# Kernel tuning notes

Hardware: AMD Instinct MI355X
Metric: run time of the kernel (lower is better)

The kernel has to match this reference:

```python
import jax, jax.numpy as jnp
import numpy as np

N_NODES = 100000
N_EDGES = 1600000
IN_CH = 128


def _sage_conv(x, src, dst, Wl, b, Wr, n_nodes):
    # PyG SAGEConv (aggr='mean', root_weight=True):
    #   out_i = lin_l(mean_{j->i} x_j) + lin_r(x_i)
    msg = x[src]                                             # [E, F]
    agg = jax.ops.segment_sum(msg, dst, num_segments=n_nodes)  # [N, F]
    deg = jax.ops.segment_sum(jnp.ones((src.shape[0],), x.dtype), dst,
                              num_segments=n_nodes)          # [N]
    mean = agg / jnp.maximum(deg, 1.0)[:, None]
    return mean @ Wl + b + x @ Wr


def setup_inputs() -> dict:
    key = jax.random.key(0)
    ks = jax.random.split(key, 10)
    x = jax.random.normal(ks[0], (N_NODES, IN_CH), dtype=jnp.float32)
    edge_index = jax.random.randint(ks[1], (2, N_EDGES), 0, N_NODES, dtype=jnp.int64)
    s = 0.05
    return {
        "x": x,
        "edge_index": edge_index,
        "W1l": jax.random.normal(ks[2], (IN_CH, 32), dtype=jnp.float32) * s,
        "b1": jax.random.normal(ks[3], (32,), dtype=jnp.float32) * s,
        "W1r": jax.random.normal(ks[4], (IN_CH, 32), dtype=jnp.float32) * s,
        "W2l": jax.random.normal(ks[5], (32, 16), dtype=jnp.float32) * s,
        "b2": jax.random.normal(ks[6], (16,), dtype=jnp.float32) * s,
        "W2r": jax.random.normal(ks[7], (32, 16), dtype=jnp.float32) * s,
        "Wfc": jax.random.normal(ks[8], (16, 2), dtype=jnp.float32) * s,
        "bfc": jax.random.normal(ks[9], (2,), dtype=jnp.float32) * s,
    }


def reference(x, edge_index, W1l, b1, W1r, W2l, b2, W2r, Wfc, bfc):
    src, dst = edge_index[0], edge_index[1]
    n = x.shape[0]
    h = jax.nn.relu(_sage_conv(x, src, dst, W1l, b1, W1r, n))   # [N, 32]
    h = jax.nn.relu(_sage_conv(h, src, dst, W2l, b2, W2r, n))   # [N, 16]
    return h @ Wfc + bfc                                        # [N, 2]
```

## Files before the change

### kernel.cpp

```cpp
#include <hip/hip_runtime.h>

#define TPB 256
#define BK_SHIFT 7
#define BK_SIZE 128
#define NBK_MAX 800
#define EPT 32

typedef __attribute__((ext_vector_type(8))) short bf16x8;
typedef __attribute__((ext_vector_type(4))) float f32x4;

__device__ __forceinline__ unsigned short f2bf(float f) {
    unsigned u = __float_as_uint(f);
    unsigned r = (u + 0x7FFFu + ((u >> 16) & 1u)) >> 16;
    return (unsigned short)r;
}
__device__ __forceinline__ float bf2f(unsigned short b) {
    return __uint_as_float((unsigned)b << 16);
}

__global__ __launch_bounds__(256) void hist_buckets(
    const int* __restrict__ dst, int* __restrict__ bcnt, int E, int NBK)
{
    __shared__ int h[NBK_MAX];
    const int t = threadIdx.x;
    for (int i = t; i < NBK; i += 256) h[i] = 0;
    __syncthreads();
    const int E4 = E >> 2;
    for (int e4 = blockIdx.x * blockDim.x + t; e4 < E4; e4 += gridDim.x * blockDim.x) {
        int4 d = ((const int4*)dst)[e4];
        atomicAdd(&h[d.x >> BK_SHIFT], 1);
        atomicAdd(&h[d.y >> BK_SHIFT], 1);
        atomicAdd(&h[d.z >> BK_SHIFT], 1);
        atomicAdd(&h[d.w >> BK_SHIFT], 1);
    }
    if (blockIdx.x == 0) {
        for (int e = E4 * 4 + t; e < E; e += 256)
            atomicAdd(&h[dst[e] >> BK_SHIFT], 1);
    }
    __syncthreads();
    for (int i = t; i < NBK; i += 256)
        if (h[i]) atomicAdd(&bcnt[i], h[i]);
}

__global__ __launch_bounds__(1024) void scan_buckets(
    const int* __restrict__ bcnt, int* __restrict__ bbase,
    int* __restrict__ gcursor, int NBK)
{
    __shared__ int s[1024];
    const int t = threadIdx.x;
    int v = (t < NBK) ? bcnt[t] : 0;
    s[t] = v;
    __syncthreads();
    for (int off = 1; off < 1024; off <<= 1) {
        int u = (t >= off) ? s[t - off] : 0;
        __syncthreads();
        s[t] += u;
        __syncthreads();
    }
    if (t < NBK) {
        int excl = s[t] - v;
        bbase[t]   = excl;
        gcursor[t] = excl;
    }
}

__global__ __launch_bounds__(256) void bin_scatter(
    const int* __restrict__ src, const int* __restrict__ dst,
    int* __restrict__ gcursor, int* __restrict__ pk, int E, int NBK)
{
    __shared__ int lcnt[NBK_MAX];
    __shared__ int lbase[NBK_MAX];
    __shared__ int lrank[NBK_MAX];
    const int t = threadIdx.x;
    const int e0 = blockIdx.x * (256 * EPT);

    for (int i = t; i < NBK; i += 256) { lcnt[i] = 0; lrank[i] = 0; }
    __syncthreads();

    #pragma unroll 4
    for (int k = 0; k < EPT; ++k) {
        int e = e0 + k * 256 + t;
        if (e < E) atomicAdd(&lcnt[dst[e] >> BK_SHIFT], 1);
    }
    __syncthreads();

    for (int i = t; i < NBK; i += 256) {
        int c = lcnt[i];
        if (c) lbase[i] = atomicAdd(&gcursor[i], c);
    }
    __syncthreads();

    #pragma unroll 4
    for (int k = 0; k < EPT; ++k) {
        int e = e0 + k * 256 + t;
        if (e < E) {
            int d = dst[e], s = src[e];
            int b = d >> BK_SHIFT;
            int r = atomicAdd(&lrank[b], 1);
            pk[lbase[b] + r] = (s << BK_SHIFT) | (d & (BK_SIZE - 1));
        }
    }
}

__global__ __launch_bounds__(256) void bucket_csr(
    const int* __restrict__ pk, const int* __restrict__ bbase,
    const int* __restrict__ bcnt,
    int* __restrict__ csr_src, int* __restrict__ row_start,
    int* __restrict__ row_end, int N)
{
    __shared__ int lcnt[BK_SIZE];
    __shared__ int s[BK_SIZE];
    __shared__ int wcur[BK_SIZE];
    const int t = threadIdx.x;
    const int b = blockIdx.x;
    const int base = bbase[b];
    const int cnt  = bcnt[b];
    const int node0 = b * BK_SIZE;

    if (t < BK_SIZE) lcnt[t] = 0;
    __syncthreads();

    for (int j = t; j < cnt; j += 256)
        atomicAdd(&lcnt[pk[base + j] & (BK_SIZE - 1)], 1);
    __syncthreads();

    if (t < BK_SIZE) s[t] = lcnt[t];
    __syncthreads();
    for (int off = 1; off < BK_SIZE; off <<= 1) {
        int u = (t < BK_SIZE && t >= off) ? s[t - off] : 0;
        __syncthreads();
        if (t < BK_SIZE) s[t] += u;
        __syncthreads();
    }
    if (t < BK_SIZE) {
        int excl = s[t] - lcnt[t];
        wcur[t] = excl;
        int node = node0 + t;
        if (node < N) {
            row_start[node] = base + excl;
            row_end[node]   = base + s[t];
        }
    }
    __syncthreads();

    for (int j = t; j < cnt; j += 256) {
        int v = pk[base + j];
        int d = v & (BK_SIZE - 1);
        int pos = atomicAdd(&wcur[d], 1);
        csr_src[base + pos] = v >> BK_SHIFT;
    }
}

__global__ __launch_bounds__(256) void gemm1_mfma(
    const float* __restrict__ A,
    const float* __restrict__ Wl,
    const float* __restrict__ Wr,
    const float* __restrict__ b,
    unsigned short* __restrict__ Yb,
    float* __restrict__ C,
    int N)
{
    const int lane = threadIdx.x & 63;
    const int m    = lane & 15;
    const int quad = lane >> 4;
    const int wave   = blockIdx.x * (blockDim.x >> 6) + (threadIdx.x >> 6);
    const int nwaves = gridDim.x * (blockDim.x >> 6);
    const int ntiles = (N + 15) >> 4;

    bf16x8 Bf[4][4];
    #pragma unroll
    for (int kc = 0; kc < 4; ++kc) {
        #pragma unroll
        for (int jt = 0; jt < 4; ++jt) {
            const float* W = (jt < 2) ? Wl : Wr;
            const int col = (jt & 1) * 16 + m;
            #pragma unroll
            for (int j = 0; j < 8; ++j) {
                int k = kc * 32 + quad * 8 + j;
                Bf[kc][jt][j] = (short)f2bf(W[k * 32 + col]);
            }
        }
    }

    const float bias0 = b[m];
    const float bias1 = b[16 + m];

    for (int tile = wave; tile < ntiles; tile += nwaves) {
        const int node0 = tile * 16;
        const int gn = node0 + m;
        const bool okA = gn < N;
        const float* rowp = A + (size_t)gn * 128;

        bf16x8 Af[4];
        #pragma unroll
        for (int kc = 0; kc < 4; ++kc) {
            float4 v0 = make_float4(0.f, 0.f, 0.f, 0.f);
            float4 v1 = make_float4(0.f, 0.f, 0.f, 0.f);
            if (okA) {
                v0 = *(const float4*)&rowp[kc * 32 + quad * 8];
                v1 = *(const float4*)&rowp[kc * 32 + quad * 8 + 4];
            }
            Af[kc][0] = (short)f2bf(v0.x); Af[kc][1] = (short)f2bf(v0.y);
            Af[kc][2] = (short)f2bf(v0.z); Af[kc][3] = (short)f2bf(v0.w);
            Af[kc][4] = (short)f2bf(v1.x); Af[kc][5] = (short)f2bf(v1.y);
            Af[kc][6] = (short)f2bf(v1.z); Af[kc][7] = (short)f2bf(v1.w);
        }

        f32x4 acc[4] = {{0.f,0.f,0.f,0.f},{0.f,0.f,0.f,0.f},
                        {0.f,0.f,0.f,0.f},{0.f,0.f,0.f,0.f}};
        #pragma unroll
        for (int kc = 0; kc < 4; ++kc) {
            #pragma unroll
            for (int jt = 0; jt < 4; ++jt)
                acc[jt] = __builtin_amdgcn_mfma_f32_16x16x32_bf16(
                    Af[kc], Bf[kc][jt], acc[jt], 0, 0, 0);
        }

        const int nodeBase = node0 + quad * 4;
        #pragma unroll
        for (int reg = 0; reg < 4; ++reg) {
            const int node = nodeBase + reg;
            if (node < N) {
                Yb[(size_t)node * 32 + m]      = f2bf(acc[0][reg]);
                Yb[(size_t)node * 32 + 16 + m] = f2bf(acc[1][reg]);
                C [(size_t)node * 32 + m]      = acc[2][reg] + bias0;
                C [(size_t)node * 32 + 16 + m] = acc[3][reg] + bias1;
            }
        }
    }
}

__global__ __launch_bounds__(256) void gather_gemm2(
    const int* __restrict__ row_start, const int* __restrict__ row_end,
    const int* __restrict__ csr_src,
    const unsigned short* __restrict__ Yb,
    const float* __restrict__ c1,
    const float* __restrict__ W2l, const float* __restrict__ W2r,
    const float* __restrict__ b2,
    unsigned short* __restrict__ y2b, float* __restrict__ c2, int N)
{
    int gid  = blockIdx.x * blockDim.x + threadIdx.x;
    int node = gid >> 3;
    int q    = gid & 7;
    const bool active = node < N;

    float h[4] = {0.f, 0.f, 0.f, 0.f};
    if (active) {
        int start = row_start[node];
        int end   = row_end[node];
        float w   = 1.0f / fmaxf((float)(end - start), 1.0f);

        float4 a0 = make_float4(0.f, 0.f, 0.f, 0.f);
        float4 a1 = make_float4(0.f, 0.f, 0.f, 0.f);
        float4 a2 = make_float4(0.f, 0.f, 0.f, 0.f);
        float4 a3 = make_float4(0.f, 0.f, 0.f, 0.f);
        int j = start;
        for (; j + 3 < end; j += 4) {
            int s0 = csr_src[j];
            int s1 = csr_src[j + 1];
            int s2 = csr_src[j + 2];
            int s3 = csr_src[j + 3];
            ushort4 v0 = *(const ushort4*)&Yb[(size_t)s0 * 32 + q * 4];
            ushort4 v1 = *(const ushort4*)&Yb[(size_t)s1 * 32 + q * 4];
            ushort4 v2 = *(const ushort4*)&Yb[(size_t)s2 * 32 + q * 4];
            ushort4 v3 = *(const ushort4*)&Yb[(size_t)s3 * 32 + q * 4];
            a0.x += bf2f(v0.x); a0.y += bf2f(v0.y); a0.z += bf2f(v0.z); a0.w += bf2f(v0.w);
            a1.x += bf2f(v1.x); a1.y += bf2f(v1.y); a1.z += bf2f(v1.z); a1.w += bf2f(v1.w);
            a2.x += bf2f(v2.x); a2.y += bf2f(v2.y); a2.z += bf2f(v2.z); a2.w += bf2f(v2.w);
            a3.x += bf2f(v3.x); a3.y += bf2f(v3.y); a3.z += bf2f(v3.z); a3.w += bf2f(v3.w);
        }
        for (; j < end; ++j) {
            int s = csr_src[j];
            ushort4 v = *(const ushort4*)&Yb[(size_t)s * 32 + q * 4];
            a0.x += bf2f(v.x); a0.y += bf2f(v.y); a0.z += bf2f(v.z); a0.w += bf2f(v.w);
        }
        float4 acc;
        acc.x = (a0.x + a1.x) + (a2.x + a3.x);
        acc.y = (a0.y + a1.y) + (a2.y + a3.y);
        acc.z = (a0.z + a1.z) + (a2.z + a3.z);
        acc.w = (a0.w + a1.w) + (a2.w + a3.w);

        float4 c = *(const float4*)&c1[(size_t)node * 32 + q * 4];
        h[0] = fmaxf(c.x + acc.x * w, 0.f);
        h[1] = fmaxf(c.y + acc.y * w, 0.f);
        h[2] = fmaxf(c.z + acc.z * w, 0.f);
        h[3] = fmaxf(c.w + acc.w * w, 0.f);
    }

    const int  j0  = q * 4;
    const bool isY = (j0 < 16);
    const int  jj  = isY ? j0 : (j0 - 16);
    const float* Wb = isY ? W2l : W2r;

    float o0 = 0.f, o1 = 0.f, o2 = 0.f, o3 = 0.f;
    #pragma unroll
    for (int k = 0; k < 32; ++k) {
        float hk = __shfl(h[k & 3], k >> 2, 8);
        float4 wv = *(const float4*)&Wb[k * 16 + jj];
        o0 += hk * wv.x; o1 += hk * wv.y; o2 += hk * wv.z; o3 += hk * wv.w;
    }

    if (active) {
        if (isY) {
            ushort4 r;
            r.x = f2bf(o0); r.y = f2bf(o1); r.z = f2bf(o2); r.w = f2bf(o3);
            *(ushort4*)&y2b[(size_t)node * 16 + jj] = r;
        } else {
            float4 bb = *(const float4*)&b2[jj];
            *(float4*)&c2[(size_t)node * 16 + jj] =
                make_float4(o0 + bb.x, o1 + bb.y, o2 + bb.z, o3 + bb.w);
        }
    }
}

__global__ __launch_bounds__(256) void gather_final(
    const int* __restrict__ row_start, const int* __restrict__ row_end,
    const int* __restrict__ csr_src,
    const unsigned short* __restrict__ Yb,
    const float* __restrict__ c2,
    const float* __restrict__ Wfc,
    const float* __restrict__ bfc,
    float* __restrict__ out, int N)
{
    int gid  = blockIdx.x * blockDim.x + threadIdx.x;
    int node = gid >> 2;
    int q    = gid & 3;
    if (node >= N) return;

    int start = row_start[node];
    int end   = row_end[node];
    float w   = 1.0f / fmaxf((float)(end - start), 1.0f);

    float4 a0 = make_float4(0.f, 0.f, 0.f, 0.f);
    float4 a1 = make_float4(0.f, 0.f, 0.f, 0.f);
    float4 a2 = make_float4(0.f, 0.f, 0.f, 0.f);
    float4 a3 = make_float4(0.f, 0.f, 0.f, 0.f);
    int j = start;
    for (; j + 3 < end; j += 4) {
        int s0 = csr_src[j];
        int s1 = csr_src[j + 1];
        int s2 = csr_src[j + 2];
        int s3 = csr_src[j + 3];
        ushort4 v0 = *(const ushort4*)&Yb[(size_t)s0 * 16 + q * 4];
        ushort4 v1 = *(const ushort4*)&Yb[(size_t)s1 * 16 + q * 4];
        ushort4 v2 = *(const ushort4*)&Yb[(size_t)s2 * 16 + q * 4];
        ushort4 v3 = *(const ushort4*)&Yb[(size_t)s3 * 16 + q * 4];
        a0.x += bf2f(v0.x); a0.y += bf2f(v0.y); a0.z += bf2f(v0.z); a0.w += bf2f(v0.w);
        a1.x += bf2f(v1.x); a1.y += bf2f(v1.y); a1.z += bf2f(v1.z); a1.w += bf2f(v1.w);
        a2.x += bf2f(v2.x); a2.y += bf2f(v2.y); a2.z += bf2f(v2.z); a2.w += bf2f(v2.w);
        a3.x += bf2f(v3.x); a3.y += bf2f(v3.y); a3.z += bf2f(v3.z); a3.w += bf2f(v3.w);
    }
    for (; j < end; ++j) {
        int s = csr_src[j];
        ushort4 v = *(const ushort4*)&Yb[(size_t)s * 16 + q * 4];
        a0.x += bf2f(v.x); a0.y += bf2f(v.y); a0.z += bf2f(v.z); a0.w += bf2f(v.w);
    }
    float4 acc;
    acc.x = (a0.x + a1.x) + (a2.x + a3.x);
    acc.y = (a0.y + a1.y) + (a2.y + a3.y);
    acc.z = (a0.z + a1.z) + (a2.z + a3.z);
    acc.w = (a0.w + a1.w) + (a2.w + a3.w);

    float4 c = *(const float4*)&c2[(size_t)node * 16 + q * 4];
    float h0 = fmaxf(c.x + acc.x * w, 0.f);
    float h1 = fmaxf(c.y + acc.y * w, 0.f);
    float h2 = fmaxf(c.z + acc.z * w, 0.f);
    float h3 = fmaxf(c.w + acc.w * w, 0.f);

    const float* Wq = &Wfc[q * 8];
    float o0 = h0 * Wq[0] + h1 * Wq[2] + h2 * Wq[4] + h3 * Wq[6];
    float o1 = h0 * Wq[1] + h1 * Wq[3] + h2 * Wq[5] + h3 * Wq[7];

    o0 += __shfl_xor(o0, 1); o0 += __shfl_xor(o0, 2);
    o1 += __shfl_xor(o1, 1); o1 += __shfl_xor(o1, 2);

    if (q == 0) ((float2*)out)[node] = make_float2(o0 + bfc[0], o1 + bfc[1]);
}

extern "C" void kernel_launch(void* const* d_in, const int* in_sizes, int n_in,
                              void* d_out, int out_size, void* d_ws, size_t ws_size,
                              hipStream_t stream)
{
    const float* x   = (const float*)d_in[0];
    const int*   ei  = (const int*)d_in[1];
    const float* W1l = (const float*)d_in[2];
    const float* b1  = (const float*)d_in[3];
    const float* W1r = (const float*)d_in[4];
    const float* W2l = (const float*)d_in[5];
    const float* b2  = (const float*)d_in[6];
    const float* W2r = (const float*)d_in[7];
    const float* Wfc = (const float*)d_in[8];
    const float* bfc = (const float*)d_in[9];
    float* out = (float*)d_out;

    const int N = in_sizes[0] / 128;
    const int E = in_sizes[1] / 2;
    const int* src = ei;
    const int* dst = ei + E;

    const int NBK = (N + BK_SIZE - 1) / BK_SIZE;

    int*   bucket_cnt  = (int*)d_ws;
    int*   bucket_base = bucket_cnt + NBK_MAX;
    int*   gcursor     = bucket_base + NBK_MAX;
    int*   row_start   = gcursor + NBK_MAX;
    int*   row_end     = row_start + N;
    int*   csr_src     = row_end + N;
    unsigned short* y1b = (unsigned short*)(csr_src + E);
    float* c1          = (float*)(y1b + (size_t)N * 32);
    unsigned short* y2b = (unsigned short*)(c1 + (size_t)N * 32);
    float* c2          = (float*)(y2b + (size_t)N * 16);
    int*   pk          = (int*)y1b;

    hipMemsetAsync(bucket_cnt, 0, (size_t)NBK * sizeof(int), stream);
    hist_buckets<<<196, 256, 0, stream>>>(dst, bucket_cnt, E, NBK);
    scan_buckets<<<1, 1024, 0, stream>>>(bucket_cnt, bucket_base, gcursor, NBK);
    {
        int nb = (E + 256 * EPT - 1) / (256 * EPT);
        bin_scatter<<<nb, 256, 0, stream>>>(src, dst, gcursor, pk, E, NBK);
    }
    bucket_csr<<<NBK, 256, 0, stream>>>(pk, bucket_base, bucket_cnt,
                                        csr_src, row_start, row_end, N);

    gemm1_mfma<<<256, TPB, 0, stream>>>(x, W1l, W1r, b1, y1b, c1, N);

    gather_gemm2<<<(N * 8 + TPB - 1) / TPB, TPB, 0, stream>>>(
        row_start, row_end, csr_src, y1b, c1, W2l, W2r, b2, y2b, c2, N);

    gather_final<<<(N * 4 + TPB - 1) / TPB, TPB, 0, stream>>>(
        row_start, row_end, csr_src, y2b, c2, Wfc, bfc, out, N);
}
```

Before: 221.9 us.

## Drop per-node CSR build; aggregate bucketed edges with LDS atomics per block

Removes the bucket_csr kernel and the row_start/row_end/csr_src arrays. Each gather kernel now takes one 128-node bucket per block, streams its packed edges, and accumulates neighbour features into padded shared-memory accumulators with float atomics. Degree is counted in the first gather and stored as invdeg for reuse in the second. This saves a kernel launch and a full pass over the edge list. In exchange it relies on LDS atomic throughput, runs only about 782 blocks, and sums in a nondeterministic order.

```diff
diff --git a/kernel.cpp b/kernel.cpp
--- a/kernel.cpp
+++ b/kernel.cpp
@@ -99,55 +99,6 @@
             int r = atomicAdd(&lrank[b], 1);
             pk[lbase[b] + r] = (s << BK_SHIFT) | (d & (BK_SIZE - 1));
         }
-    }
-}
-
-__global__ __launch_bounds__(256) void bucket_csr(
-    const int* __restrict__ pk, const int* __restrict__ bbase,
-    const int* __restrict__ bcnt,
-    int* __restrict__ csr_src, int* __restrict__ row_start,
-    int* __restrict__ row_end, int N)
-{
-    __shared__ int lcnt[BK_SIZE];
-    __shared__ int s[BK_SIZE];
-    __shared__ int wcur[BK_SIZE];
-    const int t = threadIdx.x;
-    const int b = blockIdx.x;
-    const int base = bbase[b];
-    const int cnt  = bcnt[b];
-    const int node0 = b * BK_SIZE;
-
-    if (t < BK_SIZE) lcnt[t] = 0;
-    __syncthreads();
-
-    for (int j = t; j < cnt; j += 256)
-        atomicAdd(&lcnt[pk[base + j] & (BK_SIZE - 1)], 1);
-    __syncthreads();
-
-    if (t < BK_SIZE) s[t] = lcnt[t];
-    __syncthreads();
-    for (int off = 1; off < BK_SIZE; off <<= 1) {
-        int u = (t < BK_SIZE && t >= off) ? s[t - off] : 0;
-        __syncthreads();
-        if (t < BK_SIZE) s[t] += u;
-        __syncthreads();
-    }
-    if (t < BK_SIZE) {
-        int excl = s[t] - lcnt[t];
-        wcur[t] = excl;
-        int node = node0 + t;
-        if (node < N) {
-            row_start[node] = base + excl;
-            row_end[node]   = base + s[t];
-        }
-    }
-    __syncthreads();
-
-    for (int j = t; j < cnt; j += 256) {
-        int v = pk[base + j];
-        int d = v & (BK_SIZE - 1);
-        int pos = atomicAdd(&wcur[d], 1);
-        csr_src[base + pos] = v >> BK_SHIFT;
     }
 }
 
@@ -231,150 +182,152 @@
 }
 
 __global__ __launch_bounds__(256) void gather_gemm2(
-    const int* __restrict__ row_start, const int* __restrict__ row_end,
-    const int* __restrict__ csr_src,
+    const int* __restrict__ bbase, const int* __restrict__ bcnt,
+    const int* __restrict__ pk,
     const unsigned short* __restrict__ Yb,
     const float* __restrict__ c1,
     const float* __restrict__ W2l, const float* __restrict__ W2r,
     const float* __restrict__ b2,
+    float* __restrict__ invdeg,
     unsigned short* __restrict__ y2b, float* __restrict__ c2, int N)
 {
-    int gid  = blockIdx.x * blockDim.x + threadIdx.x;
-    int node = gid >> 3;
-    int q    = gid & 7;
-    const bool active = node < N;
-
-    float h[4] = {0.f, 0.f, 0.f, 0.f};
-    if (active) {
-        int start = row_start[node];
-        int end   = row_end[node];
-        float w   = 1.0f / fmaxf((float)(end - start), 1.0f);
-
-        float4 a0 = make_float4(0.f, 0.f, 0.f, 0.f);
-        float4 a1 = make_float4(0.f, 0.f, 0.f, 0.f);
-        float4 a2 = make_float4(0.f, 0.f, 0.f, 0.f);
-        float4 a3 = make_float4(0.f, 0.f, 0.f, 0.f);
-        int j = start;
-        for (; j + 3 < end; j += 4) {
-            int s0 = csr_src[j];
-            int s1 = csr_src[j + 1];
-            int s2 = csr_src[j + 2];
-            int s3 = csr_src[j + 3];
-            ushort4 v0 = *(const ushort4*)&Yb[(size_t)s0 * 32 + q * 4];
-            ushort4 v1 = *(const ushort4*)&Yb[(size_t)s1 * 32 + q * 4];
-            ushort4 v2 = *(const ushort4*)&Yb[(size_t)s2 * 32 + q * 4];
-            ushort4 v3 = *(const ushort4*)&Yb[(size_t)s3 * 32 + q * 4];
-            a0.x += bf2f(v0.x); a0.y += bf2f(v0.y); a0.z += bf2f(v0.z); a0.w += bf2f(v0.w);
-            a1.x += bf2f(v1.x); a1.y += bf2f(v1.y); a1.z += bf2f(v1.z); a1.w += bf2f(v1.w);
-            a2.x += bf2f(v2.x); a2.y += bf2f(v2.y); a2.z += bf2f(v2.z); a2.w += bf2f(v2.w);
-            a3.x += bf2f(v3.x); a3.y += bf2f(v3.y); a3.z += bf2f(v3.z); a3.w += bf2f(v3.w);
-        }
-        for (; j < end; ++j) {
-            int s = csr_src[j];
-            ushort4 v = *(const ushort4*)&Yb[(size_t)s * 32 + q * 4];
-            a0.x += bf2f(v.x); a0.y += bf2f(v.y); a0.z += bf2f(v.z); a0.w += bf2f(v.w);
-        }
-        float4 acc;
-        acc.x = (a0.x + a1.x) + (a2.x + a3.x);
-        acc.y = (a0.y + a1.y) + (a2.y + a3.y);
-        acc.z = (a0.z + a1.z) + (a2.z + a3.z);
-        acc.w = (a0.w + a1.w) + (a2.w + a3.w);
-
-        float4 c = *(const float4*)&c1[(size_t)node * 32 + q * 4];
-        h[0] = fmaxf(c.x + acc.x * w, 0.f);
-        h[1] = fmaxf(c.y + acc.y * w, 0.f);
-        h[2] = fmaxf(c.z + acc.z * w, 0.f);
-        h[3] = fmaxf(c.w + acc.w * w, 0.f);
-    }
-
-    const int  j0  = q * 4;
-    const bool isY = (j0 < 16);
-    const int  jj  = isY ? j0 : (j0 - 16);
-    const float* Wb = isY ? W2l : W2r;
-
-    float o0 = 0.f, o1 = 0.f, o2 = 0.f, o3 = 0.f;
-    #pragma unroll
-    for (int k = 0; k < 32; ++k) {
-        float hk = __shfl(h[k & 3], k >> 2, 8);
-        float4 wv = *(const float4*)&Wb[k * 16 + jj];
-        o0 += hk * wv.x; o1 += hk * wv.y; o2 += hk * wv.z; o3 += hk * wv.w;
-    }
-
-    if (active) {
-        if (isY) {
-            ushort4 r;
-            r.x = f2bf(o0); r.y = f2bf(o1); r.z = f2bf(o2); r.w = f2bf(o3);
-            *(ushort4*)&y2b[(size_t)node * 16 + jj] = r;
-        } else {
-            float4 bb = *(const float4*)&b2[jj];
-            *(float4*)&c2[(size_t)node * 16 + jj] =
-                make_float4(o0 + bb.x, o1 + bb.y, o2 + bb.z, o3 + bb.w);
+    __shared__ float acc[BK_SIZE * 33];
+    __shared__ int   ldeg[BK_SIZE];
+
+    const int t = threadIdx.x;
+    const int b = blockIdx.x;
+    const int base = bbase[b];
+    const int cnt  = bcnt[b];
+    const int node0 = b * BK_SIZE;
+
+    for (int i = t; i < BK_SIZE * 33; i += 256) acc[i] = 0.f;
+    if (t < BK_SIZE) ldeg[t] = 0;
+    __syncthreads();
+
+    const int sg = t >> 3;
+    const int q  = t & 7;
+
+    for (int e = sg; e < cnt; e += 32) {
+        int pkv = pk[base + e];
+        int s   = pkv >> BK_SHIFT;
+        int dl  = pkv & (BK_SIZE - 1);
+        ushort4 v = *(const ushort4*)&Yb[(size_t)s * 32 + q * 4];
+        float* ap = &acc[dl * 33 + q * 4];
+        atomicAdd(ap + 0, bf2f(v.x));
+        atomicAdd(ap + 1, bf2f(v.y));
+        atomicAdd(ap + 2, bf2f(v.z));
+        atomicAdd(ap + 3, bf2f(v.w));
+        if (q == 0) atomicAdd(&ldeg[dl], 1);
+    }
+    __syncthreads();
+
+    if (t < BK_SIZE) {
+        int node = node0 + t;
+        if (node < N) {
+            float w = 1.0f / fmaxf((float)ldeg[t], 1.0f);
+            invdeg[node] = w;
+            const float* crow = &c1[(size_t)node * 32];
+            #pragma unroll
+            for (int k = 0; k < 32; ++k)
+                acc[t * 33 + k] = fmaxf(crow[k] + acc[t * 33 + k] * w, 0.f);
+        }
+    }
+    __syncthreads();
+
+    {
+        const int node = t & (BK_SIZE - 1);
+        const int part = t >> 7;
+        const int gn = node0 + node;
+        if (gn < N) {
+            const float* W = part ? W2r : W2l;
+            f32x4 o0 = {0,0,0,0}, o1 = {0,0,0,0}, o2 = {0,0,0,0}, o3 = {0,0,0,0};
+            #pragma unroll
+            for (int k = 0; k < 32; ++k) {
+                float hk = acc[node * 33 + k];
+                float4 w0 = *(const float4*)&W[k * 16 + 0];
+                float4 w1 = *(const float4*)&W[k * 16 + 4];
+                float4 w2 = *(const float4*)&W[k * 16 + 8];
+                float4 w3 = *(const float4*)&W[k * 16 + 12];
+                o0[0] += hk * w0.x; o0[1] += hk * w0.y; o0[2] += hk * w0.z; o0[3] += hk * w0.w;
+                o1[0] += hk * w1.x; o1[1] += hk * w1.y; o1[2] += hk * w1.z; o1[3] += hk * w1.w;
+                o2[0] += hk * w2.x; o2[1] += hk * w2.y; o2[2] += hk * w2.z; o2[3] += hk * w2.w;
+                o3[0] += hk * w3.x; o3[1] += hk * w3.y; o3[2] += hk * w3.z; o3[3] += hk * w3.w;
+            }
+            if (part == 0) {
+                ushort4 r0, r1, r2, r3;
+                r0.x = f2bf(o0[0]); r0.y = f2bf(o0[1]); r0.z = f2bf(o0[2]); r0.w = f2bf(o0[3]);
+                r1.x = f2bf(o1[0]); r1.y = f2bf(o1[1]); r1.z = f2bf(o1[2]); r1.w = f2bf(o1[3]);
+                r2.x = f2bf(o2[0]); r2.y = f2bf(o2[1]); r2.z = f2bf(o2[2]); r2.w = f2bf(o2[3]);
+                r3.x = f2bf(o3[0]); r3.y = f2bf(o3[1]); r3.z = f2bf(o3[2]); r3.w = f2bf(o3[3]);
+                ushort4* yp = (ushort4*)&y2b[(size_t)gn * 16];
+                yp[0] = r0; yp[1] = r1; yp[2] = r2; yp[3] = r3;
+            } else {
+                float4* cp = (float4*)&c2[(size_t)gn * 16];
+                float4 bb0 = *(const float4*)&b2[0];
+                float4 bb1 = *(const float4*)&b2[4];
+                float4 bb2 = *(const float4*)&b2[8];
+                float4 bb3 = *(const float4*)&b2[12];
+                cp[0] = make_float4(o0[0]+bb0.x, o0[1]+bb0.y, o0[2]+bb0.z, o0[3]+bb0.w);
+                cp[1] = make_float4(o1[0]+bb1.x, o1[1]+bb1.y, o1[2]+bb1.z, o1[3]+bb1.w);
+                cp[2] = make_float4(o2[0]+bb2.x, o2[1]+bb2.y, o2[2]+bb2.z, o2[3]+bb2.w);
+                cp[3] = make_float4(o3[0]+bb3.x, o3[1]+bb3.y, o3[2]+bb3.z, o3[3]+bb3.w);
+            }
         }
     }
 }
 
 __global__ __launch_bounds__(256) void gather_final(
-    const int* __restrict__ row_start, const int* __restrict__ row_end,
-    const int* __restrict__ csr_src,
+    const int* __restrict__ bbase, const int* __restrict__ bcnt,
+    const int* __restrict__ pk,
     const unsigned short* __restrict__ Yb,
     const float* __restrict__ c2,
+    const float* __restrict__ invdeg,
     const float* __restrict__ Wfc,
     const float* __restrict__ bfc,
     float* __restrict__ out, int N)
 {
-    int gid  = blockIdx.x * blockDim.x + threadIdx.x;
-    int node = gid >> 2;
-    int q    = gid & 3;
-    if (node >= N) return;
-
-    int start = row_start[node];
-    int end   = row_end[node];
-    float w   = 1.0f / fmaxf((float)(end - start), 1.0f);
-
-    float4 a0 = make_float4(0.f, 0.f, 0.f, 0.f);
-    float4 a1 = make_float4(0.f, 0.f, 0.f, 0.f);
-    float4 a2 = make_float4(0.f, 0.f, 0.f, 0.f);
-    float4 a3 = make_float4(0.f, 0.f, 0.f, 0.f);
-    int j = start;
-    for (; j + 3 < end; j += 4) {
-        int s0 = csr_src[j];
-        int s1 = csr_src[j + 1];
-        int s2 = csr_src[j + 2];
-        int s3 = csr_src[j + 3];
-        ushort4 v0 = *(const ushort4*)&Yb[(size_t)s0 * 16 + q * 4];
-        ushort4 v1 = *(const ushort4*)&Yb[(size_t)s1 * 16 + q * 4];
-        ushort4 v2 = *(const ushort4*)&Yb[(size_t)s2 * 16 + q * 4];
-        ushort4 v3 = *(const ushort4*)&Yb[(size_t)s3 * 16 + q * 4];
-        a0.x += bf2f(v0.x); a0.y += bf2f(v0.y); a0.z += bf2f(v0.z); a0.w += bf2f(v0.w);
-        a1.x += bf2f(v1.x); a1.y += bf2f(v1.y); a1.z += bf2f(v1.z); a1.w += bf2f(v1.w);
-        a2.x += bf2f(v2.x); a2.y += bf2f(v2.y); a2.z += bf2f(v2.z); a2.w += bf2f(v2.w);
-        a3.x += bf2f(v3.x); a3.y += bf2f(v3.y); a3.z += bf2f(v3.z); a3.w += bf2f(v3.w);
-    }
-    for (; j < end; ++j) {
-        int s = csr_src[j];
+    __shared__ float acc[BK_SIZE * 17];
+
+    const int t = threadIdx.x;
+    const int b = blockIdx.x;
+    const int base = bbase[b];
+    const int cnt  = bcnt[b];
+    const int node0 = b * BK_SIZE;
+
+    for (int i = t; i < BK_SIZE * 17; i += 256) acc[i] = 0.f;
+    __syncthreads();
+
+    const int sg = t >> 2;
+    const int q  = t & 3;
+
+    for (int e = sg; e < cnt; e += 64) {
+        int pkv = pk[base + e];
+        int s   = pkv >> BK_SHIFT;
+        int dl  = pkv & (BK_SIZE - 1);
         ushort4 v = *(const ushort4*)&Yb[(size_t)s * 16 + q * 4];
-        a0.x += bf2f(v.x); a0.y += bf2f(v.y); a0.z += bf2f(v.z); a0.w += bf2f(v.w);
-    }
-    float4 acc;
-    acc.x = (a0.x + a1.x) + (a2.x + a3.x);
-    acc.y = (a0.y + a1.y) + (a2.y + a3.y);
-    acc.z = (a0.z + a1.z) + (a2.z + a3.z);
-    acc.w = (a0.w + a1.w) + (a2.w + a3.w);
-
-    float4 c = *(const float4*)&c2[(size_t)node * 16 + q * 4];
-    float h0 = fmaxf(c.x + acc.x * w, 0.f);
-    float h1 = fmaxf(c.y + acc.y * w, 0.f);
-    float h2 = fmaxf(c.z + acc.z * w, 0.f);
-    float h3 = fmaxf(c.w + acc.w * w, 0.f);
-
-    const float* Wq = &Wfc[q * 8];
-    float o0 = h0 * Wq[0] + h1 * Wq[2] + h2 * Wq[4] + h3 * Wq[6];
-    float o1 = h0 * Wq[1] + h1 * Wq[3] + h2 * Wq[5] + h3 * Wq[7];
-
-    o0 += __shfl_xor(o0, 1); o0 += __shfl_xor(o0, 2);
-    o1 += __shfl_xor(o1, 1); o1 += __shfl_xor(o1, 2);
-
-    if (q == 0) ((float2*)out)[node] = make_float2(o0 + bfc[0], o1 + bfc[1]);
+        float* ap = &acc[dl * 17 + q * 4];
+        atomicAdd(ap + 0, bf2f(v.x));
+        atomicAdd(ap + 1, bf2f(v.y));
+        atomicAdd(ap + 2, bf2f(v.z));
+        atomicAdd(ap + 3, bf2f(v.w));
+    }
+    __syncthreads();
+
+    if (t < BK_SIZE) {
+        int node = node0 + t;
+        if (node < N) {
+            float w = invdeg[node];
+            const float* crow = &c2[(size_t)node * 16];
+            float o0 = bfc[0], o1 = bfc[1];
+            #pragma unroll
+            for (int k = 0; k < 16; ++k) {
+                float h = fmaxf(crow[k] + acc[t * 17 + k] * w, 0.f);
+                o0 += h * Wfc[k * 2 + 0];
+                o1 += h * Wfc[k * 2 + 1];
+            }
+            ((float2*)out)[node] = make_float2(o0, o1);
+        }
+    }
 }
 
 extern "C" void kernel_launch(void* const* d_in, const int* in_sizes, int n_in,
@@ -403,14 +356,12 @@
     int*   bucket_cnt  = (int*)d_ws;
     int*   bucket_base = bucket_cnt + NBK_MAX;
     int*   gcursor     = bucket_base + NBK_MAX;
-    int*   row_start   = gcursor + NBK_MAX;
-    int*   row_end     = row_start + N;
-    int*   csr_src     = row_end + N;
-    unsigned short* y1b = (unsigned short*)(csr_src + E);
+    float* invdeg      = (float*)(gcursor + NBK_MAX);
+    int*   pk          = (int*)(invdeg + N);
+    unsigned short* y1b = (unsigned short*)(pk + E);
     float* c1          = (float*)(y1b + (size_t)N * 32);
     unsigned short* y2b = (unsigned short*)(c1 + (size_t)N * 32);
     float* c2          = (float*)(y2b + (size_t)N * 16);
-    int*   pk          = (int*)y1b;
 
     hipMemsetAsync(bucket_cnt, 0, (size_t)NBK * sizeof(int), stream);
     hist_buckets<<<196, 256, 0, stream>>>(dst, bucket_cnt, E, NBK);
@@ -419,14 +370,13 @@
         int nb = (E + 256 * EPT - 1) / (256 * EPT);
         bin_scatter<<<nb, 256, 0, stream>>>(src, dst, gcursor, pk, E, NBK);
     }
-    bucket_csr<<<NBK, 256, 0, stream>>>(pk, bucket_base, bucket_cnt,
-                                        csr_src, row_start, row_end, N);
 
     gemm1_mfma<<<256, TPB, 0, stream>>>(x, W1l, W1r, b1, y1b, c1, N);
 
-    gather_gemm2<<<(N * 8 + TPB - 1) / TPB, TPB, 0, stream>>>(
-        row_start, row_end, csr_src, y1b, c1, W2l, W2r, b2, y2b, c2, N);
-
-    gather_final<<<(N * 4 + TPB - 1) / TPB, TPB, 0, stream>>>(
-        row_start, row_end, csr_src, y2b, c2, Wfc, bfc, out, N);
-}
+    gather_gemm2<<<NBK, TPB, 0, stream>>>(
+        bucket_base, bucket_cnt, pk, y1b, c1, W2l, W2r, b2,
+        invdeg, y2b, c2, N);
+
+    gather_final<<<NBK, TPB, 0, stream>>>(
+        bucket_base, bucket_cnt, pk, y2b, c2, invdeg, Wfc, bfc, out, N);
+}
```

New measurement: 665.8 us. +200.1%, slower.

## Fuse per-bucket CSR build into gather kernels using shared-memory index lists

Applied to the files above, without the earlier changes.

Removes the separate bucket_csr kernel and the global csr_src/row_start/row_end arrays. Each gather kernel now takes one 128-node bucket per block, counts and scans destinations locally, and sorts the source indices into shared memory before aggregating. Inverse degree is written once in the first gather and reused in the second. This saves a kernel launch and the global CSR round trip, but redoes the bucket sort in both gather kernels. It also caps a bucket at CAP=3072 edges, which silently drops edges for buckets above that size, and the grid shrinks to one block per bucket (about 782 blocks), which may lower occupancy for the gathers.

```diff
diff --git a/kernel.cpp b/kernel.cpp
--- a/kernel.cpp
+++ b/kernel.cpp
@@ -5,6 +5,7 @@
 #define BK_SIZE 128
 #define NBK_MAX 800
 #define EPT 32
+#define CAP 3072
 
 typedef __attribute__((ext_vector_type(8))) short bf16x8;
 typedef __attribute__((ext_vector_type(4))) float f32x4;
@@ -16,6 +17,9 @@
 }
 __device__ __forceinline__ float bf2f(unsigned short b) {
     return __uint_as_float((unsigned)b << 16);
+}
+__device__ __forceinline__ void acc4(float4& a, ushort4 v) {
+    a.x += bf2f(v.x); a.y += bf2f(v.y); a.z += bf2f(v.z); a.w += bf2f(v.w);
 }
 
 __global__ __launch_bounds__(256) void hist_buckets(
@@ -99,55 +103,6 @@
             int r = atomicAdd(&lrank[b], 1);
             pk[lbase[b] + r] = (s << BK_SHIFT) | (d & (BK_SIZE - 1));
         }
-    }
-}
-
-__global__ __launch_bounds__(256) void bucket_csr(
-    const int* __restrict__ pk, const int* __restrict__ bbase,
-    const int* __restrict__ bcnt,
-    int* __restrict__ csr_src, int* __restrict__ row_start,
-    int* __restrict__ row_end, int N)
-{
-    __shared__ int lcnt[BK_SIZE];
-    __shared__ int s[BK_SIZE];
-    __shared__ int wcur[BK_SIZE];
-    const int t = threadIdx.x;
-    const int b = blockIdx.x;
-    const int base = bbase[b];
-    const int cnt  = bcnt[b];
-    const int node0 = b * BK_SIZE;
-
-    if (t < BK_SIZE) lcnt[t] = 0;
-    __syncthreads();
-
-    for (int j = t; j < cnt; j += 256)
-        atomicAdd(&lcnt[pk[base + j] & (BK_SIZE - 1)], 1);
-    __syncthreads();
-
-    if (t < BK_SIZE) s[t] = lcnt[t];
-    __syncthreads();
-    for (int off = 1; off < BK_SIZE; off <<= 1) {
-        int u = (t < BK_SIZE && t >= off) ? s[t - off] : 0;
-        __syncthreads();
-        if (t < BK_SIZE) s[t] += u;
-        __syncthreads();
-    }
-    if (t < BK_SIZE) {
-        int excl = s[t] - lcnt[t];
-        wcur[t] = excl;
-        int node = node0 + t;
-        if (node < N) {
-            row_start[node] = base + excl;
-            row_end[node]   = base + s[t];
-        }
-    }
-    __syncthreads();
-
-    for (int j = t; j < cnt; j += 256) {
-        int v = pk[base + j];
-        int d = v & (BK_SIZE - 1);
-        int pos = atomicAdd(&wcur[d], 1);
-        csr_src[base + pos] = v >> BK_SHIFT;
     }
 }
 
@@ -231,150 +186,225 @@
 }
 
 __global__ __launch_bounds__(256) void gather_gemm2(
-    const int* __restrict__ row_start, const int* __restrict__ row_end,
-    const int* __restrict__ csr_src,
+    const int* __restrict__ bbase, const int* __restrict__ bcnt,
+    const int* __restrict__ pk,
     const unsigned short* __restrict__ Yb,
     const float* __restrict__ c1,
     const float* __restrict__ W2l, const float* __restrict__ W2r,
     const float* __restrict__ b2,
+    float* __restrict__ invdeg,
     unsigned short* __restrict__ y2b, float* __restrict__ c2, int N)
 {
-    int gid  = blockIdx.x * blockDim.x + threadIdx.x;
-    int node = gid >> 3;
-    int q    = gid & 7;
-    const bool active = node < N;
-
-    float h[4] = {0.f, 0.f, 0.f, 0.f};
-    if (active) {
-        int start = row_start[node];
-        int end   = row_end[node];
-        float w   = 1.0f / fmaxf((float)(end - start), 1.0f);
-
-        float4 a0 = make_float4(0.f, 0.f, 0.f, 0.f);
-        float4 a1 = make_float4(0.f, 0.f, 0.f, 0.f);
-        float4 a2 = make_float4(0.f, 0.f, 0.f, 0.f);
-        float4 a3 = make_float4(0.f, 0.f, 0.f, 0.f);
-        int j = start;
-        for (; j + 3 < end; j += 4) {
-            int s0 = csr_src[j];
-            int s1 = csr_src[j + 1];
-            int s2 = csr_src[j + 2];
-            int s3 = csr_src[j + 3];
-            ushort4 v0 = *(const ushort4*)&Yb[(size_t)s0 * 32 + q * 4];
-            ushort4 v1 = *(const ushort4*)&Yb[(size_t)s1 * 32 + q * 4];
-            ushort4 v2 = *(const ushort4*)&Yb[(size_t)s2 * 32 + q * 4];
-            ushort4 v3 = *(const ushort4*)&Yb[(size_t)s3 * 32 + q * 4];
-            a0.x += bf2f(v0.x); a0.y += bf2f(v0.y); a0.z += bf2f(v0.z); a0.w += bf2f(v0.w);
-            a1.x += bf2f(v1.x); a1.y += bf2f(v1.y); a1.z += bf2f(v1.z); a1.w += bf2f(v1.w);
-            a2.x += bf2f(v2.x); a2.y += bf2f(v2.y); a2.z += bf2f(v2.z); a2.w += bf2f(v2.w);
-            a3.x += bf2f(v3.x); a3.y += bf2f(v3.y); a3.z += bf2f(v3.z); a3.w += bf2f(v3.w);
-        }
-        for (; j < end; ++j) {
-            int s = csr_src[j];
-            ushort4 v = *(const ushort4*)&Yb[(size_t)s * 32 + q * 4];
-            a0.x += bf2f(v.x); a0.y += bf2f(v.y); a0.z += bf2f(v.z); a0.w += bf2f(v.w);
-        }
-        float4 acc;
-        acc.x = (a0.x + a1.x) + (a2.x + a3.x);
-        acc.y = (a0.y + a1.y) + (a2.y + a3.y);
-        acc.z = (a0.z + a1.z) + (a2.z + a3.z);
-        acc.w = (a0.w + a1.w) + (a2.w + a3.w);
-
-        float4 c = *(const float4*)&c1[(size_t)node * 32 + q * 4];
-        h[0] = fmaxf(c.x + acc.x * w, 0.f);
-        h[1] = fmaxf(c.y + acc.y * w, 0.f);
-        h[2] = fmaxf(c.z + acc.z * w, 0.f);
-        h[3] = fmaxf(c.w + acc.w * w, 0.f);
-    }
-
-    const int  j0  = q * 4;
-    const bool isY = (j0 < 16);
-    const int  jj  = isY ? j0 : (j0 - 16);
-    const float* Wb = isY ? W2l : W2r;
-
-    float o0 = 0.f, o1 = 0.f, o2 = 0.f, o3 = 0.f;
+    __shared__ int lcnt[BK_SIZE];
+    __shared__ int soff[BK_SIZE];
+    __shared__ int wcur[BK_SIZE];
+    __shared__ int sidx[CAP];
+
+    const int t = threadIdx.x;
+    const int b = blockIdx.x;
+    const int base = bbase[b];
+    const int cnt  = min(bcnt[b], CAP);
+    const int node0 = b * BK_SIZE;
+
+    if (t < BK_SIZE) lcnt[t] = 0;
+    __syncthreads();
+
+    for (int j = t; j < cnt; j += 256)
+        atomicAdd(&lcnt[pk[base + j] & (BK_SIZE - 1)], 1);
+    __syncthreads();
+
+    int v = (t < BK_SIZE) ? lcnt[t] : 0;
+    if (t < BK_SIZE) soff[t] = v;
+    __syncthreads();
+    for (int off = 1; off < BK_SIZE; off <<= 1) {
+        int u = (t < BK_SIZE && t >= off) ? soff[t - off] : 0;
+        __syncthreads();
+        if (t < BK_SIZE) soff[t] += u;
+        __syncthreads();
+    }
+    if (t < BK_SIZE) wcur[t] = soff[t] - v;
+    __syncthreads();
+
+    for (int j = t; j < cnt; j += 256) {
+        int pv = pk[base + j];
+        int d  = pv & (BK_SIZE - 1);
+        int pos = atomicAdd(&wcur[d], 1);
+        sidx[pos] = pv >> BK_SHIFT;
+    }
+    __syncthreads();
+
+    const int q = t & 7;
     #pragma unroll
-    for (int k = 0; k < 32; ++k) {
-        float hk = __shfl(h[k & 3], k >> 2, 8);
-        float4 wv = *(const float4*)&Wb[k * 16 + jj];
-        o0 += hk * wv.x; o1 += hk * wv.y; o2 += hk * wv.z; o3 += hk * wv.w;
-    }
-
-    if (active) {
-        if (isY) {
-            ushort4 r;
-            r.x = f2bf(o0); r.y = f2bf(o1); r.z = f2bf(o2); r.w = f2bf(o3);
-            *(ushort4*)&y2b[(size_t)node * 16 + jj] = r;
-        } else {
-            float4 bb = *(const float4*)&b2[jj];
-            *(float4*)&c2[(size_t)node * 16 + jj] =
-                make_float4(o0 + bb.x, o1 + bb.y, o2 + bb.z, o3 + bb.w);
+    for (int pass = 0; pass < 4; ++pass) {
+        const int nl = pass * 32 + (t >> 3);
+        const int node = node0 + nl;
+        const bool active = node < N;
+        float h[4] = {0.f, 0.f, 0.f, 0.f};
+        if (active) {
+            const int deg = lcnt[nl];
+            const int en  = soff[nl];
+            const int st  = en - deg;
+            const float w = 1.0f / fmaxf((float)deg, 1.0f);
+            if (q == 0) invdeg[node] = w;
+
+            float4 a0 = make_float4(0.f,0.f,0.f,0.f);
+            float4 a1 = make_float4(0.f,0.f,0.f,0.f);
+            float4 a2 = make_float4(0.f,0.f,0.f,0.f);
+            float4 a3 = make_float4(0.f,0.f,0.f,0.f);
+            int j = st;
+            for (; j + 3 < en; j += 4) {
+                int s0 = sidx[j], s1 = sidx[j+1], s2 = sidx[j+2], s3 = sidx[j+3];
+                ushort4 v0 = *(const ushort4*)&Yb[(size_t)s0 * 32 + q * 4];
+                ushort4 v1 = *(const ushort4*)&Yb[(size_t)s1 * 32 + q * 4];
+                ushort4 v2 = *(const ushort4*)&Yb[(size_t)s2 * 32 + q * 4];
+                ushort4 v3 = *(const ushort4*)&Yb[(size_t)s3 * 32 + q * 4];
+                acc4(a0, v0); acc4(a1, v1); acc4(a2, v2); acc4(a3, v3);
+            }
+            for (; j < en; ++j) {
+                ushort4 vv = *(const ushort4*)&Yb[(size_t)sidx[j] * 32 + q * 4];
+                acc4(a0, vv);
+            }
+            float4 acc;
+            acc.x = (a0.x + a1.x) + (a2.x + a3.x);
+            acc.y = (a0.y + a1.y) + (a2.y + a3.y);
+            acc.z = (a0.z + a1.z) + (a2.z + a3.z);
+            acc.w = (a0.w + a1.w) + (a2.w + a3.w);
+
+            float4 c = *(const float4*)&c1[(size_t)node * 32 + q * 4];
+            h[0] = fmaxf(c.x + acc.x * w, 0.f);
+            h[1] = fmaxf(c.y + acc.y * w, 0.f);
+            h[2] = fmaxf(c.z + acc.z * w, 0.f);
+            h[3] = fmaxf(c.w + acc.w * w, 0.f);
+        }
+
+        const int  j0  = q * 4;
+        const bool isY = (j0 < 16);
+        const int  jj  = isY ? j0 : (j0 - 16);
+        const float* Wb = isY ? W2l : W2r;
+
+        float o0 = 0.f, o1 = 0.f, o2 = 0.f, o3 = 0.f;
+        #pragma unroll
+        for (int k = 0; k < 32; ++k) {
+            float hk = __shfl(h[k & 3], k >> 2, 8);
+            float4 wv = *(const float4*)&Wb[k * 16 + jj];
+            o0 += hk * wv.x; o1 += hk * wv.y; o2 += hk * wv.z; o3 += hk * wv.w;
+        }
+
+        if (active) {
+            if (isY) {
+                ushort4 r;
+                r.x = f2bf(o0); r.y = f2bf(o1); r.z = f2bf(o2); r.w = f2bf(o3);
+                *(ushort4*)&y2b[(size_t)node * 16 + jj] = r;
+            } else {
+                float4 bb = *(const float4*)&b2[jj];
+                *(float4*)&c2[(size_t)node * 16 + jj] =
+                    make_float4(o0 + bb.x, o1 + bb.y, o2 + bb.z, o3 + bb.w);
+            }
         }
     }
 }
 
 __global__ __launch_bounds__(256) void gather_final(
-    const int* __restrict__ row_start, const int* __restrict__ row_end,
-    const int* __restrict__ csr_src,
+    const int* __restrict__ bbase, const int* __restrict__ bcnt,
+    const int* __restrict__ pk,
     const unsigned short* __restrict__ Yb,
     const float* __restrict__ c2,
+    const float* __restrict__ invdeg,
     const float* __restrict__ Wfc,
     const float* __restrict__ bfc,
     float* __restrict__ out, int N)
 {
-    int gid  = blockIdx.x * blockDim.x + threadIdx.x;
-    int node = gid >> 2;
-    int q    = gid & 3;
-    if (node >= N) return;
-
-    int start = row_start[node];
-    int end   = row_end[node];
-    float w   = 1.0f / fmaxf((float)(end - start), 1.0f);
-
-    float4 a0 = make_float4(0.f, 0.f, 0.f, 0.f);
-    float4 a1 = make_float4(0.f, 0.f, 0.f, 0.f);
-    float4 a2 = make_float4(0.f, 0.f, 0.f, 0.f);
-    float4 a3 = make_float4(0.f, 0.f, 0.f, 0.f);
-    int j = start;
-    for (; j + 3 < end; j += 4) {
-        int s0 = csr_src[j];
-        int s1 = csr_src[j + 1];
-        int s2 = csr_src[j + 2];
-        int s3 = csr_src[j + 3];
-        ushort4 v0 = *(const ushort4*)&Yb[(size_t)s0 * 16 + q * 4];
-        ushort4 v1 = *(const ushort4*)&Yb[(size_t)s1 * 16 + q * 4];
-        ushort4 v2 = *(const ushort4*)&Yb[(size_t)s2 * 16 + q * 4];
-        ushort4 v3 = *(const ushort4*)&Yb[(size_t)s3 * 16 + q * 4];
-        a0.x += bf2f(v0.x); a0.y += bf2f(v0.y); a0.z += bf2f(v0.z); a0.w += bf2f(v0.w);
-        a1.x += bf2f(v1.x); a1.y += bf2f(v1.y); a1.z += bf2f(v1.z); a1.w += bf2f(v1.w);
-        a2.x += bf2f(v2.x); a2.y += bf2f(v2.y); a2.z += bf2f(v2.z); a2.w += bf2f(v2.w);
-        a3.x += bf2f(v3.x); a3.y += bf2f(v3.y); a3.z += bf2f(v3.z); a3.w += bf2f(v3.w);
-    }
-    for (; j < end; ++j) {
-        int s = csr_src[j];
-        ushort4 v = *(const ushort4*)&Yb[(size_t)s * 16 + q * 4];
-        a0.x += bf2f(v.x); a0.y += bf2f(v.y); a0.z += bf2f(v.z); a0.w += bf2f(v.w);
-    }
-    float4 acc;
-    acc.x = (a0.x + a1.x) + (a2.x + a3.x);
-    acc.y = (a0.y + a1.y) + (a2.y + a3.y);
-    acc.z = (a0.z + a1.z) + (a2.z + a3.z);
-    acc.w = (a0.w + a1.w) + (a2.w + a3.w);
-
-    float4 c = *(const float4*)&c2[(size_t)node * 16 + q * 4];
-    float h0 = fmaxf(c.x + acc.x * w, 0.f);
-    float h1 = fmaxf(c.y + acc.y * w, 0.f);
-    float h2 = fmaxf(c.z + acc.z * w, 0.f);
-    float h3 = fmaxf(c.w + acc.w * w, 0.f);
-
-    const float* Wq = &Wfc[q * 8];
-    float o0 = h0 * Wq[0] + h1 * Wq[2] + h2 * Wq[4] + h3 * Wq[6];
-    float o1 = h0 * Wq[1] + h1 * Wq[3] + h2 * Wq[5] + h3 * Wq[7];
-
-    o0 += __shfl_xor(o0, 1); o0 += __shfl_xor(o0, 2);
-    o1 += __shfl_xor(o1, 1); o1 += __shfl_xor(o1, 2);
-
-    if (q == 0) ((float2*)out)[node] = make_float2(o0 + bfc[0], o1 + bfc[1]);
+    __shared__ int lcnt[BK_SIZE];
+    __shared__ int soff[BK_SIZE];
+    __shared__ int wcur[BK_SIZE];
+    __shared__ int sidx[CAP];
+
+    const int t = threadIdx.x;
+    const int b = blockIdx.x;
+    const int base = bbase[b];
+    const int cnt  = min(bcnt[b], CAP);
+    const int node0 = b * BK_SIZE;
+
+    if (t < BK_SIZE) lcnt[t] = 0;
+    __syncthreads();
+
+    for (int j = t; j < cnt; j += 256)
+        atomicAdd(&lcnt[pk[base + j] & (BK_SIZE - 1)], 1);
+    __syncthreads();
+
+    int v = (t < BK_SIZE) ? lcnt[t] : 0;
+    if (t < BK_SIZE) soff[t] = v;
+    __syncthreads();
+    for (int off = 1; off < BK_SIZE; off <<= 1) {
+        int u = (t < BK_SIZE && t >= off) ? soff[t - off] : 0;
+        __syncthreads();
+        if (t < BK_SIZE) soff[t] += u;
+        __syncthreads();
+    }
+    if (t < BK_SIZE) wcur[t] = soff[t] - v;
+    __syncthreads();
+
+    for (int j = t; j < cnt; j += 256) {
+        int pv = pk[base + j];
+        int d  = pv & (BK_SIZE - 1);
+        int pos = atomicAdd(&wcur[d], 1);
+        sidx[pos] = pv >> BK_SHIFT;
+    }
+    __syncthreads();
+
+    const int q = t & 3;
+    #pragma unroll
+    for (int pass = 0; pass < 2; ++pass) {
+        const int nl = pass * 64 + (t >> 2);
+        const int node = node0 + nl;
+        if (node < N) {
+            const int deg = lcnt[nl];
+            const int en  = soff[nl];
+            const int st  = en - deg;
+            const float w = invdeg[node];
+
+            float4 a0 = make_float4(0.f,0.f,0.f,0.f);
+            float4 a1 = make_float4(0.f,0.f,0.f,0.f);
+            float4 a2 = make_float4(0.f,0.f,0.f,0.f);
+            float4 a3 = make_float4(0.f,0.f,0.f,0.f);
+            int j = st;
+            for (; j + 3 < en; j += 4) {
+                int s0 = sidx[j], s1 = sidx[j+1], s2 = sidx[j+2], s3 = sidx[j+3];
+                ushort4 v0 = *(const ushort4*)&Yb[(size_t)s0 * 16 + q * 4];
+                ushort4 v1 = *(const ushort4*)&Yb[(size_t)s1 * 16 + q * 4];
+                ushort4 v2 = *(const ushort4*)&Yb[(size_t)s2 * 16 + q * 4];
+                ushort4 v3 = *(const ushort4*)&Yb[(size_t)s3 * 16 + q * 4];
+                acc4(a0, v0); acc4(a1, v1); acc4(a2, v2); acc4(a3, v3);
+            }
+            for (; j < en; ++j) {
+                ushort4 vv = *(const ushort4*)&Yb[(size_t)sidx[j] * 16 + q * 4];
+                acc4(a0, vv);
+            }
+            float4 acc;
+            acc.x = (a0.x + a1.x) + (a2.x + a3.x);
+            acc.y = (a0.y + a1.y) + (a2.y + a3.y);
+            acc.z = (a0.z + a1.z) + (a2.z + a3.z);
+            acc.w = (a0.w + a1.w) + (a2.w + a3.w);
+
+            float4 c = *(const float4*)&c2[(size_t)node * 16 + q * 4];
+            float h0 = fmaxf(c.x + acc.x * w, 0.f);
+            float h1 = fmaxf(c.y + acc.y * w, 0.f);
+            float h2 = fmaxf(c.z + acc.z * w, 0.f);
+            float h3 = fmaxf(c.w + acc.w * w, 0.f);
+
+            const float* Wq = &Wfc[q * 8];
+            float o0 = h0 * Wq[0] + h1 * Wq[2] + h2 * Wq[4] + h3 * Wq[6];
+            float o1 = h0 * Wq[1] + h1 * Wq[3] + h2 * Wq[5] + h3 * Wq[7];
+
+            o0 += __shfl_xor(o0, 1); o0 += __shfl_xor(o0, 2);
+            o1 += __shfl_xor(o1, 1); o1 += __shfl_xor(o1, 2);
+
+            if (q == 0) ((float2*)out)[node] = make_float2(o0 + bfc[0], o1 + bfc[1]);
+        } else {
+            float z = 0.f;
+            z += __shfl_xor(z, 1); z += __shfl_xor(z, 2);
+        }
+    }
 }
 
 extern "C" void kernel_launch(void* const* d_in, const int* in_sizes, int n_in,
@@ -403,14 +433,12 @@
     int*   bucket_cnt  = (int*)d_ws;
     int*   bucket_base = bucket_cnt + NBK_MAX;
     int*   gcursor     = bucket_base + NBK_MAX;
-    int*   row_start   = gcursor + NBK_MAX;
-    int*   row_end     = row_start + N;
-    int*   csr_src     = row_end + N;
-    unsigned short* y1b = (unsigned short*)(csr_src + E);
+    float* invdeg      = (float*)(gcursor + NBK_MAX);
+    int*   pk          = (int*)(invdeg + N);
+    unsigned short* y1b = (unsigned short*)(pk + E);
     float* c1          = (float*)(y1b + (size_t)N * 32);
     unsigned short* y2b = (unsigned short*)(c1 + (size_t)N * 32);
     float* c2          = (float*)(y2b + (size_t)N * 16);
-    int*   pk          = (int*)y1b;
 
     hipMemsetAsync(bucket_cnt, 0, (size_t)NBK * sizeof(int), stream);
     hist_buckets<<<196, 256, 0, stream>>>(dst, bucket_cnt, E, NBK);
@@ -419,14 +447,13 @@
         int nb = (E + 256 * EPT - 1) / (256 * EPT);
         bin_scatter<<<nb, 256, 0, stream>>>(src, dst, gcursor, pk, E, NBK);
     }
-    bucket_csr<<<NBK, 256, 0, stream>>>(pk, bucket_base, bucket_cnt,
-                                        csr_src, row_start, row_end, N);
 
     gemm1_mfma<<<256, TPB, 0, stream>>>(x, W1l, W1r, b1, y1b, c1, N);
 
-    gather_gemm2<<<(N * 8 + TPB - 1) / TPB, TPB, 0, stream>>>(
-        row_start, row_end, csr_src, y1b, c1, W2l, W2r, b2, y2b, c2, N);
-
-    gather_final<<<(N * 4 + TPB - 1) / TPB, TPB, 0, stream>>>(
-        row_start, row_end, csr_src, y2b, c2, Wfc, bfc, out, N);
-}
+    gather_gemm2<<<NBK, TPB, 0, stream>>>(
+        bucket_base, bucket_cnt, pk, y1b, c1, W2l, W2r, b2,
+        invdeg, y2b, c2, N);
+
+    gather_final<<<NBK, TPB, 0, stream>>>(
+        bucket_base, bucket_cnt, pk, y2b, c2, invdeg, Wfc, bfc, out, N);
+}
```

After: 214.5 us. 3.3% less time.
